# Optimization experiments

Measured on AMD Instinct MI355X. Metric: run time of the kernel, lower is better.

## Reference

```python
import jax, jax.numpy as jnp
import numpy as np


def _ln(x, w, b):
    m = x.mean(-1, keepdims=True)
    v = ((x - m) ** 2).mean(-1, keepdims=True)
    return (x - m) / jnp.sqrt(v + 1e-5) * w + b


def setup_inputs() -> dict:
    key = jax.random.key(0)
    ks = jax.random.split(key, 8)
    N, C, H, W = 2, 64, 128, 128
    heads, ksz = 2, 7
    C4 = 4 * C
    p = lambda k, shape: jax.random.normal(k, shape, dtype=jnp.float32) * 0.02
    return {
        "x": jax.random.normal(ks[0], (N, C, H, W), dtype=jnp.float32),
        "qkv_w": p(ks[1], (3 * C, C)),
        "qkv_b": jnp.zeros((3 * C,), jnp.float32),
        "proj_w": p(ks[2], (C, C)),
        "proj_b": jnp.zeros((C,), jnp.float32),
        "rpb": p(ks[3], (heads, 2 * ksz - 1, 2 * ksz - 1)),
        "ln1_w": jnp.ones((C,), jnp.float32),
        "ln1_b": jnp.zeros((C,), jnp.float32),
        "ln2_w": jnp.ones((C,), jnp.float32),
        "ln2_b": jnp.zeros((C,), jnp.float32),
        "fc1_w": p(ks[4], (C4, C)),
        "fc1_b": jnp.zeros((C4,), jnp.float32),
        "fc2_w": p(ks[5], (C, C4)),
        "fc2_b": jnp.zeros((C,), jnp.float32),
    }


def reference(x, qkv_w, qkv_b, proj_w, proj_b, rpb, ln1_w, ln1_b, ln2_w, ln2_b,
              fc1_w, fc1_b, fc2_w, fc2_b):
    N, C, H, W = x.shape
    heads = rpb.shape[0]
    ksz = (rpb.shape[1] + 1) // 2  # kernel size from (2k-1) bias table
    dh = C // heads

    xt = x.transpose(0, 2, 3, 1).reshape(N, H * W, C)  # n (h w) c
    shortcut = xt
    xn = _ln(xt, ln1_w, ln1_b).reshape(N, H, W, C)

    # qkv projection -> (3, N, heads, H, W, dh)
    qkv = (xn @ qkv_w.T + qkv_b).reshape(N, H, W, 3, heads, dh)
    qkv = qkv.transpose(3, 0, 4, 1, 2, 5)
    q = qkv[0] * (dh ** -0.5)
    k = qkv[1]
    v = qkv[2]

    # NATTEN neighborhood: window start clamped so every query sees k x k keys
    sh = jnp.clip(jnp.arange(H) - ksz // 2, 0, H - ksz)
    sw = jnp.clip(jnp.arange(W) - ksz // 2, 0, W - ksz)
    rows = sh[:, None] + jnp.arange(ksz)  # (H, k) key row indices
    cols = sw[:, None] + jnp.arange(ksz)  # (W, k) key col indices

    # relative position bias index: (query - key) + (k-1) in [0, 2k-2]
    rel_h = jnp.arange(H)[:, None] - rows + (ksz - 1)  # (H, k)
    rel_w = jnp.arange(W)[:, None] - cols + (ksz - 1)  # (W, k)
    bias = rpb[:, rel_h][:, :, :, rel_w]               # (heads, H, k, W, k)
    bias = bias.transpose(0, 1, 3, 2, 4)               # (heads, H, W, k, k)

    ri = rows[:, None, :, None]  # (H,1,k,1)
    ci = cols[None, :, None, :]  # (1,W,1,k)
    kwin = k[:, :, ri, ci, :]    # (N, heads, H, W, k, k, dh)
    vwin = v[:, :, ri, ci, :]

    scores = jnp.einsum('nzhwd,nzhwijd->nzhwij', q, kwin) + bias[None]
    attn = jax.nn.softmax(scores.reshape(N, heads, H, W, ksz * ksz), axis=-1)
    out = jnp.einsum('nzhwe,nzhwed->nzhwd', attn,
                     vwin.reshape(N, heads, H, W, ksz * ksz, dh))
    out = out.transpose(0, 2, 3, 1, 4).reshape(N, H, W, C) @ proj_w.T + proj_b

    x2 = shortcut + out.reshape(N, H * W, C)
    y = _ln(x2, ln2_w, ln2_b)
    y = jax.nn.gelu(y @ fc1_w.T + fc1_b, approximate=False) @ fc2_w.T + fc2_b
    x3 = x2 + y
    return x3.reshape(N, H, W, C).transpose(0, 3, 1, 2)
```

## Files before the change

kernel.cpp:

```cpp
#include <hip/hip_runtime.h>
#include <math.h>

#define TQ   32768
#define HWSZ 16384
#define CC   64
#define HH   128
#define WW   128
#define C3   192
#define C4   256
#define KS   7

typedef _Float16 half2v __attribute__((ext_vector_type(2)));
typedef _Float16 half4v __attribute__((ext_vector_type(4)));
typedef _Float16 half8v __attribute__((ext_vector_type(8)));
typedef float    f32x4  __attribute__((ext_vector_type(4)));

#define MFMA16(a, b, c) __builtin_amdgcn_mfma_f32_16x16x32_f16((a), (b), (c), 0, 0, 0)

__global__ __launch_bounds__(256) void k_qkvln(const float* __restrict__ x,
        const float* __restrict__ lnw, const float* __restrict__ lnb,
        const float* __restrict__ qw, const float* __restrict__ qb,
        const float* __restrict__ pw, const float* __restrict__ f1w,
        const float* __restrict__ f2w,
        _Float16* __restrict__ qkv16, _Float16* __restrict__ pw16,
        _Float16* __restrict__ f1w16, _Float16* __restrict__ f2w16) {
    __shared__ union {
        struct { __align__(16) _Float16 A[128 * 72]; __align__(16) _Float16 B[192 * 72]; } st;
        __align__(16) _Float16 outb[128 * 200];
    } u;
    __shared__ float ps1[256], ps2[256], m_s[128], r_s[128];
    __shared__ float w_s[64], b_s[64], bias_s[192];
    int tid = threadIdx.x;
    int t0 = blockIdx.x * 128;
    if (tid < 64) { w_s[tid] = lnw[tid]; b_s[tid] = lnb[tid]; }
    if (tid < 192) bias_s[tid] = qb[tid];
    int tok = tid & 127, cq = tid >> 7;
    int t = t0 + tok;
    int n = t >> 14, hw = t & (HWSZ - 1);
    const float* xr = x + ((size_t)n << 20) + hw;
    float v[32];
    float s = 0.f, s2 = 0.f;
#pragma unroll
    for (int e = 0; e < 32; ++e) {
        float f = xr[(cq * 32 + e) * HWSZ];
        v[e] = f; s += f; s2 += f * f;
    }
    ps1[tid] = s; ps2[tid] = s2;
    for (int i = tid; i < 3072; i += 256) {
        int jj = i >> 4, seg = i & 15;
        float4 v4 = *(const float4*)&qw[(size_t)jj * 64 + seg * 4];
        half4v h4 = { (_Float16)v4.x, (_Float16)v4.y, (_Float16)v4.z, (_Float16)v4.w };
        *(half4v*)&u.st.B[jj * 72 + seg * 4] = h4;
    }
    {
        int g = blockIdx.x * 256 + tid;
        if (g < 4096) pw16[g] = (_Float16)pw[g];
        else if (g < 20480) f1w16[g - 4096] = (_Float16)f1w[g - 4096];
        else if (g < 36864) f2w16[g - 20480] = (_Float16)f2w[g - 20480];
    }
    __syncthreads();
    if (tid < 128) {
        float ss = ps1[tid] + ps1[tid + 128];
        float qq = ps2[tid] + ps2[tid + 128];
        float m = ss * (1.f / 64.f);
        float var = qq * (1.f / 64.f) - m * m;
        m_s[tid] = m; r_s[tid] = rsqrtf(var + 1e-5f);
    }
    __syncthreads();
    {
        float m = m_s[tok], r = r_s[tok];
#pragma unroll
        for (int u8 = 0; u8 < 4; ++u8) {
            half8v o;
#pragma unroll
            for (int e = 0; e < 8; ++e) {
                int c = cq * 32 + u8 * 8 + e;
                o[e] = (_Float16)((v[u8 * 8 + e] - m) * r * w_s[c] + b_s[c]);
            }
            *(half8v*)&u.st.A[tok * 72 + cq * 32 + u8 * 8] = o;
        }
    }
    __syncthreads();
    int lane = tid & 63, wv = tid >> 6;
    int quad = lane >> 4, l16 = lane & 15;
    int mt0 = (wv & 1) * 64, nt0 = (wv >> 1) * 96;
    f32x4 acc[4][6];
#pragma unroll
    for (int mf = 0; mf < 4; ++mf)
#pragma unroll
        for (int nf = 0; nf < 6; ++nf) acc[mf][nf] = (f32x4){0.f, 0.f, 0.f, 0.f};
#pragma unroll
    for (int ks = 0; ks < 64; ks += 32) {
        half8v a[4], bfr[6];
#pragma unroll
        for (int mf = 0; mf < 4; ++mf)
            a[mf] = *(const half8v*)&u.st.A[(mt0 + mf * 16 + l16) * 72 + ks + quad * 8];
#pragma unroll
        for (int nf = 0; nf < 6; ++nf)
            bfr[nf] = *(const half8v*)&u.st.B[(nt0 + nf * 16 + l16) * 72 + ks + quad * 8];
#pragma unroll
        for (int mf = 0; mf < 4; ++mf)
#pragma unroll
            for (int nf = 0; nf < 6; ++nf) acc[mf][nf] = MFMA16(a[mf], bfr[nf], acc[mf][nf]);
    }
    __syncthreads();
    const float qscale = 0.17677669529663687f;
#pragma unroll
    for (int mf = 0; mf < 4; ++mf)
#pragma unroll
        for (int nf = 0; nf < 6; ++nf) {
            int j = nt0 + nf * 16 + l16;
            float bias = bias_s[j];
            float sc = (j < 64) ? qscale : 1.f;
#pragma unroll
            for (int r = 0; r < 4; ++r) {
                int tl = mt0 + mf * 16 + quad * 4 + r;
                u.outb[tl * 200 + j] = (_Float16)((acc[mf][nf][r] + bias) * sc);
            }
        }
    __syncthreads();
    for (int i = tid; i < 4096; i += 256) {
        int tk = i >> 5, rem = i & 31;
        if (rem < 24)
            *(half8v*)&qkv16[(size_t)(t0 + tk) * C3 + rem * 8] =
                *(const half8v*)&u.outb[tk * 200 + rem * 8];
    }
}

__global__ __launch_bounds__(256) void k_attnproj(const _Float16* __restrict__ qkv16,
        const float* __restrict__ rpb,
        const _Float16* __restrict__ pw16, const float* __restrict__ pb,
        const float* __restrict__ x,
        const float* __restrict__ ln2w, const float* __restrict__ ln2b,
        _Float16* __restrict__ x2_16, _Float16* __restrict__ xn2_16) {
    __shared__ __align__(16) char smem[77704];
    _Float16* kv_s  = (_Float16*)smem;
    _Float16* q_s   = (_Float16*)(smem + 53312);
    _Float16* s_s   = (_Float16*)(smem + 63552);
    float*    rpb_s = (float*)(smem + 76352);
    float* x2t  = (float*)smem;
    float* ps1  = (float*)(smem + 20480);
    float* ps2  = (float*)(smem + 21504);
    float* m_s  = (float*)(smem + 22528);
    float* r_s  = (float*)(smem + 22784);
    float* w_s  = (float*)(smem + 23040);
    float* b_s  = (float*)(smem + 23296);
    float* pb_s = (float*)(smem + 23552);

    int tid = threadIdx.x;
    int bx = blockIdx.x;
    int n  = bx >> 8;
    int th = (bx >> 4) & 15, tw = bx & 15;
    int h0 = th * 8, w0 = tw * 8;
    int wr0 = min(max(h0 - 3, 0), HH - 14);
    int ww0 = min(max(w0 - 3, 0), WW - 14);
    int tbase = n << 14;
    int lane = tid & 63, wvi = tid >> 6;
    int quad = lane >> 4, l16 = lane & 15;

    for (int i = tid; i < 338; i += 256) rpb_s[i] = rpb[i];
    for (int i = tid; i < 196 * 16; i += 256) {
        int tok = i >> 4, u = i & 15;
        int wi = tok / 14, wj = tok - wi * 14;
        *(half8v*)&kv_s[tok * 136 + u * 8] = *(const half8v*)&qkv16[
            (size_t)(tbase + (wr0 + wi) * WW + ww0 + wj) * C3 + 64 + u * 8];
    }
    for (int i = tid; i < 64 * 8; i += 256) {
        int q = i >> 3, u = i & 7;
        int qg = tbase + (h0 + (q >> 3)) * WW + (w0 + (q & 7));
        *(half8v*)&q_s[q * 80 + u * 8] = *(const half8v*)&qkv16[(size_t)qg * C3 + u * 8];
    }
    __syncthreads();

    int c16 = tid & 1, z = (tid >> 1) & 1, q = tid >> 2;
    int qy = q >> 3, qx = q & 7;
    int h = h0 + qy, wc = w0 + qx;
    int sh = min(max(h - 3, 0), HH - KS);
    int sw = min(max(wc - 3, 0), WW - KS);
    int oh = sh - wr0, ow = sw - ww0;
    int dhp = h - sh + 6, dwp = wc - sw + 6;
    {
        const half8v* qp = (const half8v*)&q_s[q * 80 + z * 32];
        half8v q0 = qp[0], q1 = qp[1], q2 = qp[2], q3 = qp[3];
        int i7 = 0, j7 = c16;
        for (int nb = c16; nb < 49; nb += 2) {
            int tok = (oh + i7) * 14 + (ow + j7);
            const half8v* kp = (const half8v*)&kv_s[tok * 136 + z * 32];
            half2v acc2 = { (_Float16)0.f, (_Float16)0.f };
            half8v k0 = kp[0], k1 = kp[1], k2 = kp[2], k3 = kp[3];
            acc2 += (half2v){k0.s0, k0.s1} * (half2v){q0.s0, q0.s1};
            acc2 += (half2v){k0.s2, k0.s3} * (half2v){q0.s2, q0.s3};
            acc2 += (half2v){k0.s4, k0.s5} * (half2v){q0.s4, q0.s5};
            acc2 += (half2v){k0.s6, k0.s7} * (half2v){q0.s6, q0.s7};
            acc2 += (half2v){k1.s0, k1.s1} * (half2v){q1.s0, q1.s1};
            acc2 += (half2v){k1.s2, k1.s3} * (half2v){q1.s2, q1.s3};
            acc2 += (half2v){k1.s4, k1.s5} * (half2v){q1.s4, q1.s5};
            acc2 += (half2v){k1.s6, k1.s7} * (half2v){q1.s6, q1.s7};
            acc2 += (half2v){k2.s0, k2.s1} * (half2v){q2.s0, q2.s1};
            acc2 += (half2v){k2.s2, k2.s3} * (half2v){q2.s2, q2.s3};
            acc2 += (half2v){k2.s4, k2.s5} * (half2v){q2.s4, q2.s5};
            acc2 += (half2v){k2.s6, k2.s7} * (half2v){q2.s6, q2.s7};
            acc2 += (half2v){k3.s0, k3.s1} * (half2v){q3.s0, q3.s1};
            acc2 += (half2v){k3.s2, k3.s3} * (half2v){q3.s2, q3.s3};
            acc2 += (half2v){k3.s4, k3.s5} * (half2v){q3.s4, q3.s5};
            acc2 += (half2v){k3.s6, k3.s7} * (half2v){q3.s6, q3.s7};
            float s = (float)acc2.x + (float)acc2.y
                    + rpb_s[(z * 13 + (dhp - i7)) * 13 + (dwp - j7)];
            s_s[(q * 2 + z) * 50 + nb] = (_Float16)s;
            j7 += 2;
            if (j7 >= 7) { j7 -= 7; ++i7; }
        }
    }
    __syncthreads();

    if (tid < 128) {
        _Float16* sp = &s_s[tid * 50];
        float mx = -1e30f;
        for (int i = 0; i < 49; ++i) mx = fmaxf(mx, (float)sp[i]);
        float sum = 0.f;
        for (int i = 0; i < 49; ++i) {
            float e = __expf((float)sp[i] - mx);
            sum += e;
            sp[i] = (_Float16)e;
        }
        float inv = 1.f / sum;
        for (int i = 0; i < 49; ++i) sp[i] = (_Float16)((float)sp[i] * inv);
    }
    __syncthreads();

    {
        const _Float16* pp = &s_s[(q * 2 + z) * 50];
        half2v acc[8];
#pragma unroll
        for (int j = 0; j < 8; ++j) acc[j] = (half2v){ (_Float16)0.f, (_Float16)0.f };
        int i7 = 0, j7 = 0;
        for (int nb = 0; nb < 49; ++nb) {
            int tok = (oh + i7) * 14 + (ow + j7);
            _Float16 p = pp[nb];
            half2v p2 = { p, p };
            const half8v* vp = (const half8v*)&kv_s[tok * 136 + 64 + z * 32 + c16 * 16];
            half8v v0 = vp[0], v1 = vp[1];
            acc[0] += (half2v){v0.s0, v0.s1} * p2;
            acc[1] += (half2v){v0.s2, v0.s3} * p2;
            acc[2] += (half2v){v0.s4, v0.s5} * p2;
            acc[3] += (half2v){v0.s6, v0.s7} * p2;
            acc[4] += (half2v){v1.s0, v1.s1} * p2;
            acc[5] += (half2v){v1.s2, v1.s3} * p2;
            acc[6] += (half2v){v1.s4, v1.s5} * p2;
            acc[7] += (half2v){v1.s6, v1.s7} * p2;
            ++j7;
            if (j7 == 7) { j7 = 0; ++i7; }
        }
        _Float16* op = q_s + q * 72 + z * 32 + c16 * 16;
        half8v o0 = {acc[0].x, acc[0].y, acc[1].x, acc[1].y, acc[2].x, acc[2].y, acc[3].x, acc[3].y};
        half8v o1 = {acc[4].x, acc[4].y, acc[5].x, acc[5].y, acc[6].x, acc[6].y, acc[7].x, acc[7].y};
        *(half8v*)op = o0;
        *(half8v*)(op + 8) = o1;
    }
    __syncthreads();
    for (int i = tid; i < 512; i += 256) {
        int jj = i >> 3, c8 = i & 7;
        *(half8v*)&s_s[jj * 72 + c8 * 8] = *(const half8v*)&pw16[jj * 64 + c8 * 8];
    }
    if (tid < 64) { w_s[tid] = ln2w[tid]; b_s[tid] = ln2b[tid]; pb_s[tid] = pb[tid]; }
    __syncthreads();
    {
        int mt0 = wvi * 16;
        f32x4 acc2[4];
#pragma unroll
        for (int nf = 0; nf < 4; ++nf) acc2[nf] = (f32x4){0.f, 0.f, 0.f, 0.f};
#pragma unroll
        for (int ks = 0; ks < 64; ks += 32) {
            half8v a = *(const half8v*)&q_s[(mt0 + l16) * 72 + ks + quad * 8];
            half8v bfr[4];
#pragma unroll
            for (int nf = 0; nf < 4; ++nf)
                bfr[nf] = *(const half8v*)&s_s[(nf * 16 + l16) * 72 + ks + quad * 8];
#pragma unroll
            for (int nf = 0; nf < 4; ++nf) acc2[nf] = MFMA16(a, bfr[nf], acc2[nf]);
        }
        __syncthreads();
        int tl0 = mt0 + quad * 4;
        int hwl = (h0 + (tl0 >> 3)) * WW + w0 + (tl0 & 7);
#pragma unroll
        for (int nf = 0; nf < 4; ++nf) {
            int j = nf * 16 + l16;
            float bias = pb_s[j];
            float4 rx = *(const float4*)&x[((size_t)(n * CC + j) << 14) + hwl];
#pragma unroll
            for (int r = 0; r < 4; ++r)
                x2t[(tl0 + r) * 68 + j] = acc2[nf][r] + bias + ((const float*)&rx)[r];
        }
    }
    __syncthreads();
    int tok = tid & 63, cq = tid >> 6;
    {
        float s = 0.f, s2 = 0.f;
#pragma unroll
        for (int e = 0; e < 16; ++e) {
            float f = x2t[tok * 68 + cq * 16 + e];
            s += f; s2 += f * f;
        }
        ps1[tid] = s; ps2[tid] = s2;
    }
    __syncthreads();
    if (tid < 64) {
        float ss = ps1[tid] + ps1[64 + tid] + ps1[128 + tid] + ps1[192 + tid];
        float qq = ps2[tid] + ps2[64 + tid] + ps2[128 + tid] + ps2[192 + tid];
        float m = ss * (1.f / 64.f);
        float var = qq * (1.f / 64.f) - m * m;
        m_s[tid] = m; r_s[tid] = rsqrtf(var + 1e-5f);
    }
    __syncthreads();
    {
        float m = m_s[tok], r = r_s[tok];
        int qg = tbase + (h0 + (tok >> 3)) * WW + (w0 + (tok & 7));
        half8v hv0, hv1, nv0, nv1;
#pragma unroll
        for (int e = 0; e < 8; ++e) {
            int c = cq * 16 + e;
            float f = x2t[tok * 68 + c];
            hv0[e] = (_Float16)f;
            nv0[e] = (_Float16)((f - m) * r * w_s[c] + b_s[c]);
        }
#pragma unroll
        for (int e = 0; e < 8; ++e) {
            int c = cq * 16 + 8 + e;
            float f = x2t[tok * 68 + c];
            hv1[e] = (_Float16)f;
            nv1[e] = (_Float16)((f - m) * r * w_s[c] + b_s[c]);
        }
        size_t base = (size_t)qg * 64 + cq * 16;
        *(half8v*)&x2_16[base] = hv0;  *(half8v*)&x2_16[base + 8] = hv1;
        *(half8v*)&xn2_16[base] = nv0; *(half8v*)&xn2_16[base + 8] = nv1;
    }
}

__global__ __launch_bounds__(512, 1) void k_mlp(const _Float16* __restrict__ xn2,
        const _Float16* __restrict__ x2_16,
        const _Float16* __restrict__ f1w16, const float* __restrict__ f1b,
        const _Float16* __restrict__ f2w16, const float* __restrict__ f2b,
        float* __restrict__ out) {
    __shared__ __align__(16) _Float16 W1[256 * 72];
    __shared__ __align__(16) _Float16 W2[64 * 264];
    __shared__ __align__(16) _Float16 A_s[64 * 72];
    __shared__ union {
        __align__(16) _Float16 H[64 * 264];
        float tr[64 * 68];
    } u;
    __shared__ float f1b_s[256], f2b_s[64];
    int tid = threadIdx.x;
    int lane = tid & 63, wv = tid >> 6;
    int quad = lane >> 4, l16 = lane & 15;
    for (int i = tid; i < 2048; i += 512) {
        int jj = i >> 3, c8 = i & 7;
        *(half8v*)&W1[jj * 72 + c8 * 8] = *(const half8v*)&f1w16[(size_t)jj * 64 + c8 * 8];
    }
    for (int i = tid; i < 2048; i += 512) {
        int jj = i >> 5, c8 = i & 31;
        *(half8v*)&W2[jj * 264 + c8 * 8] = *(const half8v*)&f2w16[(size_t)jj * 256 + c8 * 8];
    }
    if (tid < 256) f1b_s[tid] = f1b[tid];
    else if (tid < 320) f2b_s[tid - 256] = f2b[tid - 256];

    for (int tt = 0; tt < 2; ++tt) {
        int t0 = blockIdx.x * 128 + tt * 64;
        {
            int tok = tid >> 3, u8 = tid & 7;
            *(half8v*)&A_s[tok * 72 + u8 * 8] =
                *(const half8v*)&xn2[(size_t)(t0 + tok) * 64 + u8 * 8];
        }
        __syncthreads();
        {
            int mt0 = (wv & 1) * 32, nt0 = (wv >> 1) * 64;
            f32x4 acc[2][4];
#pragma unroll
            for (int mf = 0; mf < 2; ++mf)
#pragma unroll
                for (int nf = 0; nf < 4; ++nf) acc[mf][nf] = (f32x4){0.f, 0.f, 0.f, 0.f};
#pragma unroll
            for (int ks = 0; ks < 64; ks += 32) {
                half8v a[2], bfr[4];
#pragma unroll
                for (int mf = 0; mf < 2; ++mf)
                    a[mf] = *(const half8v*)&A_s[(mt0 + mf * 16 + l16) * 72 + ks + quad * 8];
#pragma unroll
                for (int nf = 0; nf < 4; ++nf)
                    bfr[nf] = *(const half8v*)&W1[(nt0 + nf * 16 + l16) * 72 + ks + quad * 8];
#pragma unroll
                for (int mf = 0; mf < 2; ++mf)
#pragma unroll
                    for (int nf = 0; nf < 4; ++nf) acc[mf][nf] = MFMA16(a[mf], bfr[nf], acc[mf][nf]);
            }
#pragma unroll
            for (int mf = 0; mf < 2; ++mf)
#pragma unroll
                for (int nf = 0; nf < 4; ++nf) {
                    int jl = nt0 + nf * 16 + l16;
                    float bias = f1b_s[jl];
#pragma unroll
                    for (int r = 0; r < 4; ++r) {
                        int tl = mt0 + mf * 16 + quad * 4 + r;
                        float vv = acc[mf][nf][r] + bias;
                        float g = 0.5f * vv * (1.f + erff(vv * 0.70710678118654752f));
                        u.H[tl * 264 + jl] = (_Float16)g;
                    }
                }
        }
        __syncthreads();
        {
            int mt = (wv & 3) * 16, n0 = (wv >> 2) * 32;
            f32x4 acc2[2];
#pragma unroll
            for (int nf = 0; nf < 2; ++nf) acc2[nf] = (f32x4){0.f, 0.f, 0.f, 0.f};
#pragma unroll
            for (int ks = 0; ks < 256; ks += 32) {
                half8v a = *(const half8v*)&u.H[(mt + l16) * 264 + ks + quad * 8];
                half8v bfr[2];
#pragma unroll
                for (int nf = 0; nf < 2; ++nf)
                    bfr[nf] = *(const half8v*)&W2[(n0 + nf * 16 + l16) * 264 + ks + quad * 8];
#pragma unroll
                for (int nf = 0; nf < 2; ++nf) acc2[nf] = MFMA16(a, bfr[nf], acc2[nf]);
            }
            __syncthreads();
#pragma unroll
            for (int nf = 0; nf < 2; ++nf) {
                int j = n0 + nf * 16 + l16;
                float bias = f2b_s[j];
#pragma unroll
                for (int r = 0; r < 4; ++r) {
                    int tl = mt + quad * 4 + r;
                    float v = acc2[nf][r] + bias + (float)x2_16[(size_t)(t0 + tl) * 64 + j];
                    u.tr[j * 68 + tl] = v;
                }
            }
        }
        __syncthreads();
        {
            int n = t0 >> 14, hw0 = t0 & (HWSZ - 1);
            for (int i = tid; i < 1024; i += 512) {
                int j = i >> 4, seg = i & 15;
                float4 v = *(const float4*)&u.tr[j * 68 + seg * 4];
                *(float4*)&out[((size_t)(n * CC + j) << 14) + hw0 + seg * 4] = v;
            }
        }
        __syncthreads();
    }
}

extern "C" void kernel_launch(void* const* d_in, const int* in_sizes, int n_in,
                              void* d_out, int out_size, void* d_ws, size_t ws_size,
                              hipStream_t stream) {
    const float* x      = (const float*)d_in[0];
    const float* qkv_w  = (const float*)d_in[1];
    const float* qkv_b  = (const float*)d_in[2];
    const float* proj_w = (const float*)d_in[3];
    const float* proj_b = (const float*)d_in[4];
    const float* rpb    = (const float*)d_in[5];
    const float* ln1_w  = (const float*)d_in[6];
    const float* ln1_b  = (const float*)d_in[7];
    const float* ln2_w  = (const float*)d_in[8];
    const float* ln2_b  = (const float*)d_in[9];
    const float* fc1_w  = (const float*)d_in[10];
    const float* fc1_b  = (const float*)d_in[11];
    const float* fc2_w  = (const float*)d_in[12];
    const float* fc2_b  = (const float*)d_in[13];
    float* out = (float*)d_out;
    char* ws = (char*)d_ws;

    _Float16* qkv16  = (_Float16*)(ws);
    _Float16* x2_16  = (_Float16*)(ws + 12582912);
    _Float16* xn2_16 = (_Float16*)(ws + 16777216);
    _Float16* pw16   = (_Float16*)(ws + 20971520);
    _Float16* f1w16  = (_Float16*)(ws + 20979712);
    _Float16* f2w16  = (_Float16*)(ws + 21012480);

    k_qkvln   <<<256, 256, 0, stream>>>(x, ln1_w, ln1_b, qkv_w, qkv_b,
                                        proj_w, fc1_w, fc2_w,
                                        qkv16, pw16, f1w16, f2w16);
    k_attnproj<<<512, 256, 0, stream>>>(qkv16, rpb, pw16, proj_b, x, ln2_w, ln2_b,
                                        x2_16, xn2_16);
    k_mlp     <<<256, 512, 0, stream>>>(xn2_16, x2_16, f1w16, fc1_b, f2w16, fc2_b, out);
}
```

Before: 130.8 us.

## Fuse MLP into attention kernel and defer softmax normalization

```diff
diff --git a/kernel.cpp b/kernel.cpp
--- a/kernel.cpp
+++ b/kernel.cpp
@@ -16,6 +16,12 @@
 typedef float    f32x4  __attribute__((ext_vector_type(4)));
 
 #define MFMA16(a, b, c) __builtin_amdgcn_mfma_f32_16x16x32_f16((a), (b), (c), 0, 0, 0)
+
+__device__ __forceinline__ float gelu_f(float v) {
+    float z = v * (1.59576912f + 0.07135481f * v * v);
+    float e = __expf(-z);
+    return v * (1.f / (1.f + e));
+}
 
 __global__ __launch_bounds__(256) void k_qkvln(const float* __restrict__ x,
         const float* __restrict__ lnw, const float* __restrict__ lnb,
@@ -127,17 +133,20 @@
     }
 }
 
-__global__ __launch_bounds__(256) void k_attnproj(const _Float16* __restrict__ qkv16,
+__global__ __launch_bounds__(256) void k_attn_mlp(const _Float16* __restrict__ qkv16,
         const float* __restrict__ rpb,
         const _Float16* __restrict__ pw16, const float* __restrict__ pb,
         const float* __restrict__ x,
         const float* __restrict__ ln2w, const float* __restrict__ ln2b,
-        _Float16* __restrict__ x2_16, _Float16* __restrict__ xn2_16) {
-    __shared__ __align__(16) char smem[77704];
+        const _Float16* __restrict__ f1w16, const float* __restrict__ f1b,
+        const _Float16* __restrict__ f2w16, const float* __restrict__ f2b,
+        float* __restrict__ out) {
+    __shared__ __align__(16) char smem[78216];
     _Float16* kv_s  = (_Float16*)smem;
     _Float16* q_s   = (_Float16*)(smem + 53312);
     _Float16* s_s   = (_Float16*)(smem + 63552);
     float*    rpb_s = (float*)(smem + 76352);
+    float*    sum_s = (float*)(smem + 77704);
     float* x2t  = (float*)smem;
     float* ps1  = (float*)(smem + 20480);
     float* ps2  = (float*)(smem + 21504);
@@ -146,6 +155,11 @@
     float* w_s  = (float*)(smem + 23040);
     float* b_s  = (float*)(smem + 23296);
     float* pb_s = (float*)(smem + 23552);
+    _Float16* A2_s = (_Float16*)(smem + 53312);
+    _Float16* H_s  = (_Float16*)(smem + 17408);
+    float*    tr_s = (float*)(smem + 17408);
+    float*    f1b_s = (float*)(smem + 63552);
+    float*    f2b_s = (float*)(smem + 64576);
 
     int tid = threadIdx.x;
     int bx = blockIdx.x;
@@ -223,8 +237,7 @@
             sum += e;
             sp[i] = (_Float16)e;
         }
-        float inv = 1.f / sum;
-        for (int i = 0; i < 49; ++i) sp[i] = (_Float16)((float)sp[i] * inv);
+        sum_s[tid] = 1.f / sum;
     }
     __syncthreads();
 
@@ -251,9 +264,16 @@
             ++j7;
             if (j7 == 7) { j7 = 0; ++i7; }
         }
+        float inv = sum_s[q * 2 + z];
         _Float16* op = q_s + q * 72 + z * 32 + c16 * 16;
-        half8v o0 = {acc[0].x, acc[0].y, acc[1].x, acc[1].y, acc[2].x, acc[2].y, acc[3].x, acc[3].y};
-        half8v o1 = {acc[4].x, acc[4].y, acc[5].x, acc[5].y, acc[6].x, acc[6].y, acc[7].x, acc[7].y};
+        half8v o0, o1;
+#pragma unroll
+        for (int j = 0; j < 4; ++j) {
+            o0[2 * j]     = (_Float16)((float)acc[j].x * inv);
+            o0[2 * j + 1] = (_Float16)((float)acc[j].y * inv);
+            o1[2 * j]     = (_Float16)((float)acc[4 + j].x * inv);
+            o1[2 * j + 1] = (_Float16)((float)acc[4 + j].y * inv);
+        }
         *(half8v*)op = o0;
         *(half8v*)(op + 8) = o1;
     }
@@ -292,6 +312,8 @@
                 x2t[(tl0 + r) * 68 + j] = acc2[nf][r] + bias + ((const float*)&rx)[r];
         }
     }
+    f1b_s[tid] = f1b[tid];
+    if (tid < 64) f2b_s[tid] = f2b[tid];
     __syncthreads();
     int tok = tid & 63, cq = tid >> 6;
     {
@@ -314,138 +336,92 @@
     __syncthreads();
     {
         float m = m_s[tok], r = r_s[tok];
-        int qg = tbase + (h0 + (tok >> 3)) * WW + (w0 + (tok & 7));
-        half8v hv0, hv1, nv0, nv1;
+        half8v nv0, nv1;
 #pragma unroll
         for (int e = 0; e < 8; ++e) {
             int c = cq * 16 + e;
             float f = x2t[tok * 68 + c];
-            hv0[e] = (_Float16)f;
             nv0[e] = (_Float16)((f - m) * r * w_s[c] + b_s[c]);
         }
 #pragma unroll
         for (int e = 0; e < 8; ++e) {
             int c = cq * 16 + 8 + e;
             float f = x2t[tok * 68 + c];
-            hv1[e] = (_Float16)f;
             nv1[e] = (_Float16)((f - m) * r * w_s[c] + b_s[c]);
         }
-        size_t base = (size_t)qg * 64 + cq * 16;
-        *(half8v*)&x2_16[base] = hv0;  *(half8v*)&x2_16[base + 8] = hv1;
-        *(half8v*)&xn2_16[base] = nv0; *(half8v*)&xn2_16[base + 8] = nv1;
-    }
-}
-
-__global__ __launch_bounds__(512, 1) void k_mlp(const _Float16* __restrict__ xn2,
-        const _Float16* __restrict__ x2_16,
-        const _Float16* __restrict__ f1w16, const float* __restrict__ f1b,
-        const _Float16* __restrict__ f2w16, const float* __restrict__ f2b,
-        float* __restrict__ out) {
-    __shared__ __align__(16) _Float16 W1[256 * 72];
-    __shared__ __align__(16) _Float16 W2[64 * 264];
-    __shared__ __align__(16) _Float16 A_s[64 * 72];
-    __shared__ union {
-        __align__(16) _Float16 H[64 * 264];
-        float tr[64 * 68];
-    } u;
-    __shared__ float f1b_s[256], f2b_s[64];
-    int tid = threadIdx.x;
-    int lane = tid & 63, wv = tid >> 6;
-    int quad = lane >> 4, l16 = lane & 15;
-    for (int i = tid; i < 2048; i += 512) {
-        int jj = i >> 3, c8 = i & 7;
-        *(half8v*)&W1[jj * 72 + c8 * 8] = *(const half8v*)&f1w16[(size_t)jj * 64 + c8 * 8];
-    }
-    for (int i = tid; i < 2048; i += 512) {
-        int jj = i >> 5, c8 = i & 31;
-        *(half8v*)&W2[jj * 264 + c8 * 8] = *(const half8v*)&f2w16[(size_t)jj * 256 + c8 * 8];
-    }
-    if (tid < 256) f1b_s[tid] = f1b[tid];
-    else if (tid < 320) f2b_s[tid - 256] = f2b[tid - 256];
-
-    for (int tt = 0; tt < 2; ++tt) {
-        int t0 = blockIdx.x * 128 + tt * 64;
-        {
-            int tok = tid >> 3, u8 = tid & 7;
-            *(half8v*)&A_s[tok * 72 + u8 * 8] =
-                *(const half8v*)&xn2[(size_t)(t0 + tok) * 64 + u8 * 8];
-        }
-        __syncthreads();
-        {
-            int mt0 = (wv & 1) * 32, nt0 = (wv >> 1) * 64;
-            f32x4 acc[2][4];
-#pragma unroll
-            for (int mf = 0; mf < 2; ++mf)
-#pragma unroll
-                for (int nf = 0; nf < 4; ++nf) acc[mf][nf] = (f32x4){0.f, 0.f, 0.f, 0.f};
-#pragma unroll
-            for (int ks = 0; ks < 64; ks += 32) {
-                half8v a[2], bfr[4];
-#pragma unroll
-                for (int mf = 0; mf < 2; ++mf)
-                    a[mf] = *(const half8v*)&A_s[(mt0 + mf * 16 + l16) * 72 + ks + quad * 8];
-#pragma unroll
-                for (int nf = 0; nf < 4; ++nf)
-                    bfr[nf] = *(const half8v*)&W1[(nt0 + nf * 16 + l16) * 72 + ks + quad * 8];
-#pragma unroll
-                for (int mf = 0; mf < 2; ++mf)
-#pragma unroll
-                    for (int nf = 0; nf < 4; ++nf) acc[mf][nf] = MFMA16(a[mf], bfr[nf], acc[mf][nf]);
-            }
-#pragma unroll
-            for (int mf = 0; mf < 2; ++mf)
-#pragma unroll
-                for (int nf = 0; nf < 4; ++nf) {
-                    int jl = nt0 + nf * 16 + l16;
-                    float bias = f1b_s[jl];
-#pragma unroll
-                    for (int r = 0; r < 4; ++r) {
-                        int tl = mt0 + mf * 16 + quad * 4 + r;
-                        float vv = acc[mf][nf][r] + bias;
-                        float g = 0.5f * vv * (1.f + erff(vv * 0.70710678118654752f));
-                        u.H[tl * 264 + jl] = (_Float16)g;
-                    }
-                }
-        }
-        __syncthreads();
-        {
-            int mt = (wv & 3) * 16, n0 = (wv >> 2) * 32;
-            f32x4 acc2[2];
-#pragma unroll
-            for (int nf = 0; nf < 2; ++nf) acc2[nf] = (f32x4){0.f, 0.f, 0.f, 0.f};
-#pragma unroll
-            for (int ks = 0; ks < 256; ks += 32) {
-                half8v a = *(const half8v*)&u.H[(mt + l16) * 264 + ks + quad * 8];
-                half8v bfr[2];
-#pragma unroll
-                for (int nf = 0; nf < 2; ++nf)
-                    bfr[nf] = *(const half8v*)&W2[(n0 + nf * 16 + l16) * 264 + ks + quad * 8];
-#pragma unroll
-                for (int nf = 0; nf < 2; ++nf) acc2[nf] = MFMA16(a, bfr[nf], acc2[nf]);
-            }
-            __syncthreads();
-#pragma unroll
-            for (int nf = 0; nf < 2; ++nf) {
-                int j = n0 + nf * 16 + l16;
-                float bias = f2b_s[j];
+        *(half8v*)&A2_s[tok * 72 + cq * 16] = nv0;
+        *(half8v*)&A2_s[tok * 72 + cq * 16 + 8] = nv1;
+    }
+    __syncthreads();
+    {
+        int nt0 = wvi * 64;
+        f32x4 acc[4][4];
+#pragma unroll
+        for (int mf = 0; mf < 4; ++mf)
+#pragma unroll
+            for (int nf = 0; nf < 4; ++nf) acc[mf][nf] = (f32x4){0.f, 0.f, 0.f, 0.f};
+#pragma unroll
+        for (int ks = 0; ks < 64; ks += 32) {
+            half8v a[4], bfr[4];
+#pragma unroll
+            for (int mf = 0; mf < 4; ++mf)
+                a[mf] = *(const half8v*)&A2_s[(mf * 16 + l16) * 72 + ks + quad * 8];
+#pragma unroll
+            for (int nf = 0; nf < 4; ++nf)
+                bfr[nf] = *(const half8v*)&f1w16[(size_t)(nt0 + nf * 16 + l16) * 64 + ks + quad * 8];
+#pragma unroll
+            for (int mf = 0; mf < 4; ++mf)
+#pragma unroll
+                for (int nf = 0; nf < 4; ++nf) acc[mf][nf] = MFMA16(a[mf], bfr[nf], acc[mf][nf]);
+        }
+#pragma unroll
+        for (int mf = 0; mf < 4; ++mf)
+#pragma unroll
+            for (int nf = 0; nf < 4; ++nf) {
+                int jl = nt0 + nf * 16 + l16;
+                float bias = f1b_s[jl];
 #pragma unroll
                 for (int r = 0; r < 4; ++r) {
-                    int tl = mt + quad * 4 + r;
-                    float v = acc2[nf][r] + bias + (float)x2_16[(size_t)(t0 + tl) * 64 + j];
-                    u.tr[j * 68 + tl] = v;
+                    int tl = mf * 16 + quad * 4 + r;
+                    H_s[tl * 264 + jl] = (_Float16)gelu_f(acc[mf][nf][r] + bias);
                 }
             }
+    }
+    __syncthreads();
+    {
+        int mt = wvi * 16;
+        f32x4 acc2[4];
+#pragma unroll
+        for (int nf = 0; nf < 4; ++nf) acc2[nf] = (f32x4){0.f, 0.f, 0.f, 0.f};
+#pragma unroll
+        for (int ks = 0; ks < 256; ks += 32) {
+            half8v a = *(const half8v*)&H_s[(mt + l16) * 264 + ks + quad * 8];
+            half8v bfr[4];
+#pragma unroll
+            for (int nf = 0; nf < 4; ++nf)
+                bfr[nf] = *(const half8v*)&f2w16[(size_t)(nf * 16 + l16) * 256 + ks + quad * 8];
+#pragma unroll
+            for (int nf = 0; nf < 4; ++nf) acc2[nf] = MFMA16(a, bfr[nf], acc2[nf]);
         }
         __syncthreads();
-        {
-            int n = t0 >> 14, hw0 = t0 & (HWSZ - 1);
-            for (int i = tid; i < 1024; i += 512) {
-                int j = i >> 4, seg = i & 15;
-                float4 v = *(const float4*)&u.tr[j * 68 + seg * 4];
-                *(float4*)&out[((size_t)(n * CC + j) << 14) + hw0 + seg * 4] = v;
+#pragma unroll
+        for (int nf = 0; nf < 4; ++nf) {
+            int j = nf * 16 + l16;
+            float bias = f2b_s[j];
+#pragma unroll
+            for (int r = 0; r < 4; ++r) {
+                int tl = mt + quad * 4 + r;
+                float v = acc2[nf][r] + bias + x2t[tl * 68 + j];
+                tr_s[j * 68 + tl] = v;
             }
         }
-        __syncthreads();
+    }
+    __syncthreads();
+    for (int i = tid; i < 2048; i += 256) {
+        int j = i >> 5, tl = (i & 31) * 2;
+        *(float2*)&out[((size_t)(n * CC + j) << 14)
+                       + (size_t)((h0 + (tl >> 3)) * WW + w0 + (tl & 7))] =
+            *(const float2*)&tr_s[j * 68 + tl];
     }
 }
 
@@ -470,8 +446,6 @@
     char* ws = (char*)d_ws;
 
     _Float16* qkv16  = (_Float16*)(ws);
-    _Float16* x2_16  = (_Float16*)(ws + 12582912);
-    _Float16* xn2_16 = (_Float16*)(ws + 16777216);
     _Float16* pw16   = (_Float16*)(ws + 20971520);
     _Float16* f1w16  = (_Float16*)(ws + 20979712);
     _Float16* f2w16  = (_Float16*)(ws + 21012480);
@@ -479,7 +453,6 @@
     k_qkvln   <<<256, 256, 0, stream>>>(x, ln1_w, ln1_b, qkv_w, qkv_b,
                                         proj_w, fc1_w, fc2_w,
                                         qkv16, pw16, f1w16, f2w16);
-    k_attnproj<<<512, 256, 0, stream>>>(qkv16, rpb, pw16, proj_b, x, ln2_w, ln2_b,
-                                        x2_16, xn2_16);
-    k_mlp     <<<256, 512, 0, stream>>>(xn2_16, x2_16, f1w16, fc1_b, f2w16, fc2_b, out);
+    k_attn_mlp<<<512, 256, 0, stream>>>(qkv16, rpb, pw16, proj_b, x, ln2_w, ln2_b,
+                                        f1w16, fc1_b, f2w16, fc2_b, out);
 }
```

New measurement: 125.9 us. -3.8%, faster.
